# Performance work log

Measured on AMD Instinct MI355X. Metric: run time of the kernel, lower is better.

## Reference

```python
import jax, jax.numpy as jnp
import numpy as np
import math

B, S, D, NCLS, H = 32, 2048, 512, 2, 16
HD = D // H
KSIZE = 19


def setup_inputs() -> dict:
    key = jax.random.key(0)
    ks = jax.random.split(key, 20)
    f32 = jnp.float32
    s = 1.0 / math.sqrt(D)
    inp = {}
    inp['x'] = jax.random.normal(ks[0], (B, S, D), dtype=f32)
    # wave params [2, D, 1]: row 0 = scale (1 + randn), row 1 = shift
    inp['wave1'] = jnp.concatenate([1.0 + jax.random.normal(ks[1], (1, D, 1), f32), jax.random.normal(ks[2], (1, D, 1), f32)], axis=0)
    inp['wave2'] = jnp.concatenate([1.0 + jax.random.normal(ks[3], (1, D, 1), f32), jnp.zeros((1, D, 1), f32)], axis=0)
    inp['wave3'] = jnp.concatenate([1.0 + jax.random.normal(ks[4], (1, D, 1), f32), jnp.zeros((1, D, 1), f32)], axis=0)
    inp['Wp1'] = jax.random.normal(ks[5], (D, D), f32) * s   # WaveletEncoding.proj_1
    inp['bp1'] = jnp.zeros((D,), f32)
    inp['cls_token'] = jax.random.normal(ks[6], (1, NCLS, D), f32) * 0.02
    inp['ln1_g'] = jnp.ones((D,), f32)
    inp['ln1_b'] = jnp.zeros((D,), f32)
    inp['Wq'] = jax.random.normal(ks[7], (D, D), f32) * s      # no bias (qkv_bias=False)
    inp['Wkv'] = jax.random.normal(ks[8], (D, 2 * D), f32) * s
    inp['Wproj'] = jax.random.normal(ks[9], (D, D), f32) * s
    inp['bproj'] = jnp.zeros((D,), f32)
    inp['ln2_g'] = jnp.ones((D,), f32)
    inp['ln2_b'] = jnp.zeros((D,), f32)
    inp['Wc1'] = jax.random.normal(ks[10], (D, D), f32) * s
    inp['bc1'] = jnp.zeros((D,), f32)
    inp['Wc2'] = jax.random.normal(ks[11], (D, 1), f32) * s
    inp['bc2'] = jnp.zeros((1,), f32)
    return inp


def _layernorm(x, g, b, eps=1e-5):
    m = jnp.mean(x, axis=-1, keepdims=True)
    v = jnp.mean((x - m) ** 2, axis=-1, keepdims=True)
    return (x - m) / jnp.sqrt(v + eps) * g + b


def _mexican_hat(wave):
    # wave: [2, D, 1] -> kernel [D, KSIZE]
    scale, shift = wave[0], wave[1]                      # [D, 1]
    half = (KSIZE - 1) // 2
    xs = jnp.linspace(-half, half, KSIZE, dtype=jnp.float32)  # [KSIZE]
    xg = xs[None, :] - shift                             # [D, KSIZE]
    C = 2.0 / (3.0 ** 0.5 * np.pi ** 0.25)
    u = xg / scale
    return C * (1.0 - u ** 2) * jnp.exp(-0.5 * u ** 2) / jnp.sqrt(jnp.abs(scale))


def _dwconv(xc, kern):
    # xc [B, D, S], kern [D, KSIZE]; depthwise 'same' conv (groups=D)
    return jax.lax.conv_general_dilated(
        xc, kern[:, None, :], window_strides=(1,), padding='SAME',
        dimension_numbers=('NCH', 'OIH', 'NCH'), feature_group_count=D)


def _forward(x, wave1, wave2, wave3, Wp1, bp1, cls_token, ln1_g, ln1_b,
             Wq, Wkv, Wproj, bproj, ln2_g, ln2_b, Wc1, bc1, Wc2, bc2):
    # Wavelet positional encoding
    xc = jnp.transpose(x, (0, 2, 1))                     # [B, D, S]
    pos = _dwconv(xc, _mexican_hat(wave1)) + _dwconv(xc, _mexican_hat(wave2)) + _dwconv(xc, _mexican_hat(wave3))
    x = x + jnp.transpose(pos, (0, 2, 1)) @ Wp1 + bp1    # [B, S, D]
    # MIL pooling: layernorm on encoder tokens, sigmoid cross-attention
    xn = _layernorm(x, ln1_g, ln1_b)
    cls = jnp.broadcast_to(cls_token, (x.shape[0], NCLS, D))
    q = (cls @ Wq).reshape(-1, NCLS, H, HD).transpose(0, 2, 1, 3)        # [B, H, N, hd]
    kv = (xn @ Wkv).reshape(-1, S, 2, H, HD).transpose(2, 0, 3, 1, 4)    # [2, B, H, S, hd]
    k, v = kv[0], kv[1]
    scale = HD ** (-0.5)
    scores = jnp.einsum('bhnd,bhsd->bhns', q, k) * scale - math.log(S)   # -log(S) bias
    attn = jax.nn.sigmoid(scores)                                        # sigmoid, not softmax
    o = jnp.einsum('bhns,bhsd->bhnd', attn, v).transpose(0, 2, 1, 3).reshape(-1, NCLS, D)
    o = o @ Wproj + bproj
    # classifier head
    h = jax.nn.relu(_layernorm(o, ln2_g, ln2_b) @ Wc1 + bc1)
    logits = (h @ Wc2 + bc2)[..., 0]                                     # [B, NCLS]
    return logits, attn


def reference(x, wave1, wave2, wave3, Wp1, bp1, cls_token, ln1_g, ln1_b,
              Wq, Wkv, Wproj, bproj, ln2_g, ln2_b, Wc1, bc1, Wc2, bc2):
    return _forward(x, wave1, wave2, wave3, Wp1, bp1, cls_token, ln1_g, ln1_b,
                    Wq, Wkv, Wproj, bproj, ln2_g, ln2_b, Wc1, bc1, Wc2, bc2)
```

## Files before the change

### kernel.cpp

```cpp
#include <hip/hip_runtime.h>

#define SEQ 2048
#define DIM 512
#define NBATCH 32
#define NH 16
#define HDIM 32
#define NCLS 2

typedef __attribute__((ext_vector_type(8))) short short8;
typedef __attribute__((ext_vector_type(8))) unsigned short ushort8;
typedef __attribute__((ext_vector_type(4))) float f32x4;

__device__ __forceinline__ float b2f(unsigned short u){
  union { unsigned int i; float f; } v; v.i = ((unsigned int)u) << 16; return v.f;
}
__device__ __forceinline__ unsigned short f2b(float f){
  unsigned int x = __float_as_uint(f);
  unsigned int r = (x + 0x7fffu + ((x >> 16) & 1u)) >> 16;
  return (unsigned short)r;
}
__device__ __forceinline__ void gload16(const void* g, void* l){
  __builtin_amdgcn_global_load_lds((const __attribute__((address_space(1))) void*)g,
                                   (__attribute__((address_space(3))) void*)l, 16, 0, 0);
}

__global__ __launch_bounds__(256) void prep1_kernel(
    const float* __restrict__ w1, const float* __restrict__ w2, const float* __restrict__ w3,
    float* __restrict__ ksum,
    const float* __restrict__ cls, const float* __restrict__ Wq, float* __restrict__ qws,
    const float* __restrict__ Wp1, unsigned short* __restrict__ Wp1T,
    const float* __restrict__ Wkv, const float* __restrict__ g1, unsigned short* __restrict__ GvT){
  __shared__ unsigned short t[64][65];
  int bid = blockIdx.x;
  int tid = threadIdx.x;
  if (bid < 2){
    int d = bid * 256 + tid;
    const float C = 0.86732501f;
    float acc[19];
    #pragma unroll
    for (int i = 0; i < 19; ++i) acc[i] = 0.f;
    const float* waves[3] = { w1, w2, w3 };
    for (int tt = 0; tt < 3; ++tt){
      float scale = waves[tt][d];
      float shift = waves[tt][DIM + d];
      float inv = 1.f / scale;
      float amp = C * rsqrtf(fabsf(scale));
      #pragma unroll
      for (int i = 0; i < 19; ++i){
        float u = ((float)(i - 9) - shift) * inv;
        acc[i] += amp * (1.f - u * u) * expf(-0.5f * u * u);
      }
    }
    #pragma unroll
    for (int i = 0; i < 19; ++i) ksum[i * DIM + d] = acc[i];
  } else if (bid < 6){
    int idx = (bid - 2) * 256 + tid;
    int n = idx >> 9, c = idx & 511;
    float s = 0.f;
    for (int kd = 0; kd < DIM; ++kd)
      s = fmaf(cls[n * DIM + kd], Wq[(size_t)kd * DIM + c], s);
    qws[n * DIM + c] = s;
  } else if (bid < 70){
    int bx = bid - 6;
    int c0 = (bx & 7) * 64, r0 = (bx >> 3) * 64;
    #pragma unroll
    for (int i = 0; i < 16; ++i){
      int idx = i * 256 + tid;
      int r = idx >> 6, c = idx & 63;
      t[c][r] = f2b(Wp1[(size_t)(r0 + r) * 512 + c0 + c]);
    }
    __syncthreads();
    #pragma unroll
    for (int i = 0; i < 16; ++i){
      int idx = i * 256 + tid;
      int r = idx >> 6, c = idx & 63;
      Wp1T[(size_t)(c0 + r) * 512 + r0 + c] = t[r][c];
    }
  } else {
    int bx = bid - 70;
    int c0 = (bx & 7) * 64, r0 = (bx >> 3) * 64;
    #pragma unroll
    for (int i = 0; i < 16; ++i){
      int idx = i * 256 + tid;
      int r = idx >> 6, c = idx & 63;
      t[c][r] = f2b(Wkv[(size_t)(r0 + r) * 1024 + 512 + c0 + c] * g1[r0 + r]);
    }
    __syncthreads();
    #pragma unroll
    for (int i = 0; i < 16; ++i){
      int idx = i * 256 + tid;
      int r = idx >> 6, c = idx & 63;
      GvT[(size_t)(c0 + r) * 512 + r0 + c] = t[r][c];
    }
  }
}

__global__ __launch_bounds__(256) void prep2_kernel(const float* __restrict__ Wkv,
    const float* __restrict__ qws, const float* __restrict__ g1, const float* __restrict__ b1,
    unsigned short* __restrict__ AqT, float* __restrict__ gv, float* __restrict__ bv,
    float* __restrict__ ga, float* __restrict__ ba){
  const float SCALE = 0.17677669529663687f;
  const float LOGS  = 7.6246189861593985f;
  int bid = blockIdx.x;
  int tid = threadIdx.x;
  if (bid < 64){
    int idx = bid * 256 + tid;
    int hn = idx >> 9, d = idx & 511;
    int h = hn >> 1, n = hn & 1;
    float s = 0.f;
    #pragma unroll
    for (int hd = 0; hd < 32; ++hd)
      s = fmaf(Wkv[(size_t)d * 1024 + h * 32 + hd], qws[n * 512 + h * 32 + hd], s);
    AqT[hn * 512 + d] = f2b(SCALE * g1[d] * s);
  } else if (bid < 96){
    __shared__ float red[64];
    int hn = bid - 64;
    int h = hn >> 1, n = hn & 1;
    float s1 = 0.f, s2 = 0.f;
    #pragma unroll
    for (int dd = 0; dd < 2; ++dd){
      int d = tid + dd * 256;
      float inner = 0.f;
      #pragma unroll
      for (int hd = 0; hd < 32; ++hd)
        inner = fmaf(Wkv[(size_t)d * 1024 + h * 32 + hd], qws[n * 512 + h * 32 + hd], inner);
      s1 = fmaf(g1[d], inner, s1);
      s2 = fmaf(b1[d], inner, s2);
    }
    #pragma unroll
    for (int off = 32; off; off >>= 1){
      s1 += __shfl_xor(s1, off, 64);
      s2 += __shfl_xor(s2, off, 64);
    }
    int w = tid >> 6, lane = tid & 63;
    if (lane == 0){ red[w * 2] = s1; red[w * 2 + 1] = s2; }
    __syncthreads();
    if (tid == 0){
      float t1 = red[0] + red[2] + red[4] + red[6];
      float t2 = red[1] + red[3] + red[5] + red[7];
      ga[hn] = SCALE * t1;
      ba[hn] = SCALE * t2 - LOGS;
    }
  } else {
    int c = (bid - 96) * 256 + tid;
    float s1 = 0.f, s2 = 0.f;
    for (int d = 0; d < 512; ++d){
      float wv = Wkv[(size_t)d * 1024 + 512 + c];
      s1 = fmaf(g1[d], wv, s1);
      s2 = fmaf(b1[d], wv, s2);
    }
    gv[c] = s1; bv[c] = s2;
  }
}

__global__ __launch_bounds__(256) void conv_kernel(const float* __restrict__ X,
    const float* __restrict__ ksum, unsigned short* __restrict__ Pos){
  __shared__ float xs[34 * 256];
  int id = blockIdx.x;
  int id2 = (id & 7) * 1024 + (id >> 3);
  int b = id2 >> 8;
  int rem = id2 & 255;
  int strip = rem >> 1, half = rem & 1;
  int s0 = strip * 16, c0 = half * 256;
  int tid = threadIdx.x;
  const float* xb = X + ((size_t)b * SEQ) * DIM + c0;
  #pragma unroll
  for (int i = 0; i < 9; ++i){
    int g = i * 256 + tid;
    if (g < 2176){
      int row = g >> 6;
      int gc = g & 63;
      int s = s0 - 9 + row;
      int sc = s < 0 ? 0 : (s > SEQ - 1 ? SEQ - 1 : s);
      gload16(xb + (size_t)sc * DIM + gc * 4, &xs[row * 256 + gc * 4]);
    }
  }
  __syncthreads();
  if (strip == 0){
    #pragma unroll
    for (int i = 0; i < 9; ++i) xs[i * 256 + tid] = 0.f;
    __syncthreads();
  } else if (strip == 127){
    #pragma unroll
    for (int i = 25; i < 34; ++i) xs[i * 256 + tid] = 0.f;
    __syncthreads();
  }
  int d = tid;
  float kx[19];
  #pragma unroll
  for (int t = 0; t < 19; ++t) kx[t] = ksum[t * DIM + c0 + d];
  float ox[16];
  #pragma unroll
  for (int o = 0; o < 16; ++o) ox[o] = 0.f;
  #pragma unroll
  for (int w = 0; w < 34; ++w){
    float xv = xs[w * 256 + d];
    #pragma unroll
    for (int o = 0; o < 16; ++o){
      int t2 = w - o;
      if (t2 >= 0 && t2 < 19) ox[o] = fmaf(xv, kx[t2], ox[o]);
    }
  }
  #pragma unroll
  for (int o = 0; o < 16; ++o)
    Pos[((size_t)(b * SEQ + s0 + o)) * DIM + c0 + d] = f2b(ox[o]);
}

__global__ __launch_bounds__(512, 4) void gemm1_kernel(const unsigned short* __restrict__ A,
    const unsigned short* __restrict__ Bt, const float* __restrict__ Xres,
    const float* __restrict__ bias, unsigned short* __restrict__ Out,
    float* __restrict__ stat_part){
  __shared__ unsigned short lA[2 * 8192];
  __shared__ unsigned short lB[2 * 8192];
  __shared__ float sred[128][2][2];
  int tid = threadIdx.x;
  int w = tid >> 6, lane = tid & 63;
  int wm = w >> 1, wn = w & 1;
  int q = lane >> 4, cl = lane & 15;
  int id = blockIdx.x;
  int xcd = id & 7;
  int nch = (id >> 3) & 3;
  int mb  = ((id >> 5) << 3) | xcd;
  size_t mBase = (size_t)mb * 128;
  int nBase = nch * 128;

  auto stage = [&](int buf, int k0){
    #pragma unroll
    for (int p = 0; p < 2; ++p){
      int G = p * 512 + tid;
      int row = G >> 3;
      int c8 = (G & 7) ^ (row & 7);
      gload16(A + (mBase + row) * 512 + k0 + c8 * 8, &lA[buf * 8192 + G * 8]);
      gload16(Bt + (size_t)(nBase + row) * 512 + k0 + c8 * 8, &lB[buf * 8192 + G * 8]);
    }
  };

  f32x4 acc[2][4] = {};
  stage(0, 0);
  __syncthreads();
  int cur = 0;
  #pragma unroll
  for (int t = 0; t < 8; ++t){
    if (t < 7){
      stage(cur ^ 1, (t + 1) * 64);
      asm volatile("s_waitcnt vmcnt(4)" ::: "memory");
    } else {
      asm volatile("s_waitcnt vmcnt(0)" ::: "memory");
    }
    __builtin_amdgcn_s_barrier();
    const unsigned short* cA = &lA[cur * 8192];
    const unsigned short* cB = &lB[cur * 8192];
    #pragma unroll
    for (int kk = 0; kk < 2; ++kk){
      short8 af[2], bfr[4];
      #pragma unroll
      for (int m = 0; m < 2; ++m){
        int row = wm * 32 + m * 16 + cl;
        af[m] = *(const short8*)&cA[row * 64 + (((kk * 4 + q) ^ (row & 7)) * 8)];
      }
      #pragma unroll
      for (int n = 0; n < 4; ++n){
        int row = wn * 64 + n * 16 + cl;
        bfr[n] = *(const short8*)&cB[row * 64 + (((kk * 4 + q) ^ (row & 7)) * 8)];
      }
      #pragma unroll
      for (int m = 0; m < 2; ++m){
        #pragma unroll
        for (int n = 0; n < 4; ++n)
          acc[m][n] = __builtin_amdgcn_mfma_f32_16x16x32_bf16(af[m], bfr[n], acc[m][n], 0, 0, 0);
      }
    }
    asm volatile("s_waitcnt lgkmcnt(0)" ::: "memory");
    __builtin_amdgcn_s_barrier();
    cur ^= 1;
  }
  #pragma unroll
  for (int m = 0; m < 2; ++m){
    #pragma unroll
    for (int j = 0; j < 4; ++j){
      int rl = wm * 32 + m * 16 + q * 4 + j;
      size_t row = mBase + rl;
      float sm = 0.f, sq = 0.f;
      #pragma unroll
      for (int n = 0; n < 4; ++n){
        int col = nBase + wn * 64 + n * 16 + cl;
        float v = acc[m][n][j] + Xres[row * DIM + col] + bias[col];
        Out[row * DIM + col] = f2b(v);
        sm += v; sq += v * v;
      }
      #pragma unroll
      for (int off = 1; off < 16; off <<= 1){
        sm += __shfl_xor(sm, off, 64);
        sq += __shfl_xor(sq, off, 64);
      }
      if (cl == 0){ sred[rl][wn][0] = sm; sred[rl][wn][1] = sq; }
    }
  }
  __syncthreads();
  if (tid < 128){
    float sm = sred[tid][0][0] + sred[tid][1][0];
    float sq = sred[tid][0][1] + sred[tid][1][1];
    stat_part[((mBase + tid) * 4 + nch) * 2 + 0] = sm;
    stat_part[((mBase + tid) * 4 + nch) * 2 + 1] = sq;
  }
}

__global__ __launch_bounds__(512, 4) void stage2_kernel(
    const unsigned short* __restrict__ Y, const unsigned short* __restrict__ GvT,
    const unsigned short* __restrict__ AqT, const float* __restrict__ stat_part,
    const float* __restrict__ gv, const float* __restrict__ bv,
    const float* __restrict__ ga, const float* __restrict__ ba,
    float* __restrict__ aout, float* __restrict__ o_part){
  __shared__ __align__(16) char smem[74752];
  unsigned short* lA = (unsigned short*)smem;
  unsigned short* lB = (unsigned short*)(smem + 32768);
  float* stats = (float*)(smem + 73728);
  float* attn_lds = (float*)smem;
  float* o_red = (float*)(smem + 16896);
  int tid = threadIdx.x;
  int w = tid >> 6, lane = tid & 63;
  int wm = w >> 1, wn = w & 1;
  int q = lane >> 4, cl = lane & 15;
  int id = blockIdx.x;
  int xcd = id & 7;
  int nch = (id >> 3) & 3;
  int mb  = ((id >> 5) << 3) | xcd;
  size_t mBase = (size_t)mb * 128;
  int nBase = nch * 128;

  auto stage = [&](int buf, int k0){
    #pragma unroll
    for (int p = 0; p < 2; ++p){
      int G = p * 512 + tid;
      int row = G >> 3;
      int c8 = (G & 7) ^ (row & 7);
      gload16(Y + (mBase + row) * 512 + k0 + c8 * 8, &lA[buf * 8192 + G * 8]);
      gload16(GvT + (size_t)(nBase + row) * 512 + k0 + c8 * 8, &lB[buf * 10240 + G * 8]);
    }
    {
      int g = tid & 255;
      int row = 128 + (g >> 3);
      int c8 = (g & 7) ^ (row & 7);
      gload16(AqT + (size_t)(row - 128) * 512 + k0 + c8 * 8, &lB[buf * 10240 + (1024 + g) * 8]);
    }
  };

  stage(0, 0);
  if (tid < 128){
    float sm = 0.f, sq = 0.f;
    #pragma unroll
    for (int i = 0; i < 4; ++i){
      sm += stat_part[((mBase + tid) * 4 + i) * 2 + 0];
      sq += stat_part[((mBase + tid) * 4 + i) * 2 + 1];
    }
    float mean = sm * (1.f / 512.f);
    float var = sq * (1.f / 512.f) - mean * mean;
    stats[tid * 2 + 0] = mean;
    stats[tid * 2 + 1] = rsqrtf(var + 1e-5f);
  }
  __syncthreads();

  int hn = wn * 16 + cl;
  f32x4 acc[2][4] = {};
  f32x4 accs[2] = {};
  int cur = 0;
  #pragma unroll
  for (int t = 0; t < 8; ++t){
    if (t < 7){
      stage(cur ^ 1, (t + 1) * 64);
      asm volatile("s_waitcnt vmcnt(5)" ::: "memory");
    } else {
      asm volatile("s_waitcnt vmcnt(0)" ::: "memory");
    }
    __builtin_amdgcn_s_barrier();
    const unsigned short* cA = &lA[cur * 8192];
    const unsigned short* cB = &lB[cur * 10240];
    #pragma unroll
    for (int kk = 0; kk < 2; ++kk){
      short8 af[2], bfr[4], bq;
      {
        int row = 128 + hn;
        bq = *(const short8*)&cB[row * 64 + (((kk * 4 + q) ^ (row & 7)) * 8)];
      }
      #pragma unroll
      for (int m = 0; m < 2; ++m){
        int row = wm * 32 + m * 16 + cl;
        af[m] = *(const short8*)&cA[row * 64 + (((kk * 4 + q) ^ (row & 7)) * 8)];
      }
      #pragma unroll
      for (int n = 0; n < 4; ++n){
        int row = wn * 64 + n * 16 + cl;
        bfr[n] = *(const short8*)&cB[row * 64 + (((kk * 4 + q) ^ (row & 7)) * 8)];
      }
      #pragma unroll
      for (int m = 0; m < 2; ++m){
        #pragma unroll
        for (int n = 0; n < 4; ++n)
          acc[m][n] = __builtin_amdgcn_mfma_f32_16x16x32_bf16(af[m], bfr[n], acc[m][n], 0, 0, 0);
        accs[m] = __builtin_amdgcn_mfma_f32_16x16x32_bf16(af[m], bq, accs[m], 0, 0, 0);
      }
    }
    asm volatile("s_waitcnt lgkmcnt(0)" ::: "memory");
    __builtin_amdgcn_s_barrier();
    cur ^= 1;
  }
  float gav = ga[hn], bav = ba[hn];
  float gv4[4], bv4[4];
  #pragma unroll
  for (int n = 0; n < 4; ++n){
    int cg = nBase + wn * 64 + n * 16 + cl;
    gv4[n] = gv[cg]; bv4[n] = bv[cg];
  }
  int b = mb >> 4;
  int scb = (mb & 15) * 128;
  #pragma unroll
  for (int m = 0; m < 2; ++m){
    #pragma unroll
    for (int j = 0; j < 4; ++j){
      int rl = wm * 32 + m * 16 + q * 4 + j;
      float mu = stats[rl * 2 + 0], s = stats[rl * 2 + 1];
      float sc = s * accs[m][j] - s * mu * gav + bav;
      float at = 1.f / (1.f + expf(-sc));
      attn_lds[rl * 33 + hn] = at;
      if (nch == 0)
        aout[((size_t)(b * NH + (hn >> 1)) * NCLS + (hn & 1)) * SEQ + scb + rl] = at;
      #pragma unroll
      for (int n = 0; n < 4; ++n)
        acc[m][n][j] = s * acc[m][n][j] - s * mu * gv4[n] + bv4[n];
    }
  }
  __syncthreads();
  float o0[4] = {}, o1[4] = {};
  #pragma unroll
  for (int n = 0; n < 4; ++n){
    int cg = nBase + wn * 64 + n * 16 + cl;
    int h2 = ((cg >> 5) << 1);
    #pragma unroll
    for (int m = 0; m < 2; ++m){
      #pragma unroll
      for (int j = 0; j < 4; ++j){
        int rl = wm * 32 + m * 16 + q * 4 + j;
        float vv = acc[m][n][j];
        o0[n] = fmaf(attn_lds[rl * 33 + h2 + 0], vv, o0[n]);
        o1[n] = fmaf(attn_lds[rl * 33 + h2 + 1], vv, o1[n]);
      }
    }
  }
  #pragma unroll
  for (int n = 0; n < 4; ++n){
    o0[n] += __shfl_xor(o0[n], 16, 64);
    o0[n] += __shfl_xor(o0[n], 32, 64);
    o1[n] += __shfl_xor(o1[n], 16, 64);
    o1[n] += __shfl_xor(o1[n], 32, 64);
  }
  if (q == 0){
    #pragma unroll
    for (int n = 0; n < 4; ++n){
      int c = wn * 64 + n * 16 + cl;
      o_red[(0 * 4 + wm) * 128 + c] = o0[n];
      o_red[(1 * 4 + wm) * 128 + c] = o1[n];
    }
  }
  __syncthreads();
  if (tid < 256){
    int nn = tid >> 7, c = tid & 127;
    float v = o_red[(nn * 4 + 0) * 128 + c] + o_red[(nn * 4 + 1) * 128 + c]
            + o_red[(nn * 4 + 2) * 128 + c] + o_red[(nn * 4 + 3) * 128 + c];
    o_part[((size_t)mb * 2 + nn) * 512 + nBase + c] = v;
  }
}

__global__ __launch_bounds__(256) void head_kernel(const float* __restrict__ o_part,
    const float* __restrict__ Wproj, const float* __restrict__ bproj,
    const float* __restrict__ g2, const float* __restrict__ b2v,
    const float* __restrict__ Wc1, const float* __restrict__ bc1,
    const float* __restrict__ Wc2, const float* __restrict__ bc2,
    float* __restrict__ logits){
  __shared__ float orow[512];
  __shared__ float hrow[512];
  __shared__ float wred[8];
  __shared__ float wred2[4];
  int tid = threadIdx.x;
  int row = blockIdx.x;
  int b = row >> 1, nn = row & 1;
  for (int i = tid; i < 512; i += 256){
    float s = 0.f;
    const float* op = o_part + (((size_t)b * 16) * 2 + nn) * 512 + i;
    #pragma unroll
    for (int sc = 0; sc < 16; ++sc) s += op[(size_t)sc * 1024];
    orow[i] = s;
  }
  __syncthreads();
  int c0 = tid * 2;
  float a0 = 0.f, a1 = 0.f;
  for (int dd = 0; dd < DIM; ++dd){
    float ov = orow[dd];
    const float* wr = Wproj + (size_t)dd * DIM + c0;
    a0 = fmaf(ov, wr[0], a0);
    a1 = fmaf(ov, wr[1], a1);
  }
  a0 += bproj[c0]; a1 += bproj[c0 + 1];
  float sm = a0 + a1, sq = a0 * a0 + a1 * a1;
  #pragma unroll
  for (int off = 32; off; off >>= 1){
    sm += __shfl_xor(sm, off, 64);
    sq += __shfl_xor(sq, off, 64);
  }
  int w = tid >> 6, lane = tid & 63;
  if (lane == 0){ wred[w * 2] = sm; wred[w * 2 + 1] = sq; }
  __syncthreads();
  sm = wred[0] + wred[2] + wred[4] + wred[6];
  sq = wred[1] + wred[3] + wred[5] + wred[7];
  float mean = sm * (1.f / 512.f);
  float var = sq * (1.f / 512.f) - mean * mean;
  float rstd = rsqrtf(var + 1e-5f);
  hrow[c0]     = (a0 - mean) * rstd * g2[c0]     + b2v[c0];
  hrow[c0 + 1] = (a1 - mean) * rstd * g2[c0 + 1] + b2v[c0 + 1];
  __syncthreads();
  float h0 = 0.f, h1 = 0.f;
  for (int dd = 0; dd < DIM; ++dd){
    float lv = hrow[dd];
    const float* wr = Wc1 + (size_t)dd * DIM + c0;
    h0 = fmaf(lv, wr[0], h0);
    h1 = fmaf(lv, wr[1], h1);
  }
  h0 += bc1[c0]; h1 += bc1[c0 + 1];
  h0 = h0 > 0.f ? h0 : 0.f;
  h1 = h1 > 0.f ? h1 : 0.f;
  float p = h0 * Wc2[c0] + h1 * Wc2[c0 + 1];
  #pragma unroll
  for (int off = 32; off; off >>= 1) p += __shfl_xor(p, off, 64);
  if (lane == 0) wred2[w] = p;
  __syncthreads();
  if (tid == 0) logits[row] = wred2[0] + wred2[1] + wred2[2] + wred2[3] + bc2[0];
}

extern "C" void kernel_launch(void* const* d_in, const int* in_sizes, int n_in,
                              void* d_out, int out_size, void* d_ws, size_t ws_size,
                              hipStream_t stream) {
  const float* x     = (const float*)d_in[0];
  const float* wave1 = (const float*)d_in[1];
  const float* wave2 = (const float*)d_in[2];
  const float* wave3 = (const float*)d_in[3];
  const float* Wp1   = (const float*)d_in[4];
  const float* bp1   = (const float*)d_in[5];
  const float* cls   = (const float*)d_in[6];
  const float* ln1g  = (const float*)d_in[7];
  const float* ln1b  = (const float*)d_in[8];
  const float* Wq    = (const float*)d_in[9];
  const float* Wkv   = (const float*)d_in[10];
  const float* Wproj = (const float*)d_in[11];
  const float* bproj = (const float*)d_in[12];
  const float* ln2g  = (const float*)d_in[13];
  const float* ln2b  = (const float*)d_in[14];
  const float* Wc1   = (const float*)d_in[15];
  const float* bc1   = (const float*)d_in[16];
  const float* Wc2   = (const float*)d_in[17];
  const float* bc2   = (const float*)d_in[18];

  float* out = (float*)d_out;
  float* logits = out;
  float* attn   = out + 64;

  unsigned char* ws = (unsigned char*)d_ws;
  float* ksum           = (float*)(ws);
  float* qws            = (float*)(ws + (64u << 10));
  unsigned short* Wp1T  = (unsigned short*)(ws + (128u << 10));
  unsigned short* GvT   = (unsigned short*)(ws + (640u << 10));
  unsigned short* AqT   = (unsigned short*)(ws + (1152u << 10));
  float* gv             = (float*)(ws + (1248u << 10));
  float* bv             = (float*)(ws + (1252u << 10));
  float* ga             = (float*)(ws + (1256u << 10));
  float* ba             = (float*)(ws + (1260u << 10));
  float* o_part         = (float*)(ws + (1776u << 10));
  float* stat_part      = (float*)(ws + (4096u << 10));
  unsigned short* pos   = (unsigned short*)(ws + (8ull << 20));
  unsigned short* yb    = (unsigned short*)(ws + (72ull << 20));

  prep1_kernel<<<dim3(134), dim3(256), 0, stream>>>(wave1, wave2, wave3, ksum,
                                                    cls, Wq, qws, Wp1, Wp1T, Wkv, ln1g, GvT);
  prep2_kernel<<<dim3(98), dim3(256), 0, stream>>>(Wkv, qws, ln1g, ln1b, AqT, gv, bv, ga, ba);
  conv_kernel<<<dim3(8192), dim3(256), 0, stream>>>(x, ksum, pos);
  gemm1_kernel<<<dim3(2048), dim3(512), 0, stream>>>(pos, Wp1T, x, bp1, yb, stat_part);
  stage2_kernel<<<dim3(2048), dim3(512), 0, stream>>>(yb, GvT, AqT, stat_part,
                                                      gv, bv, ga, ba, attn, o_part);
  head_kernel<<<dim3(64), dim3(256), 0, stream>>>(o_part, Wproj, bproj, ln2g, ln2b,
                                                  Wc1, bc1, Wc2, bc2, logits);
}
```

Measured before the change: 271.2 us.

## Merge prep kernels and compute wavelet taps inside conv kernel

Folds the two preparation kernels into one launch. Each attention block now recomputes its own 32-element slice of the cls·Wq query instead of waiting for a separate kernel to write it. The wavelet kernel taps are now computed per thread inside the conv kernel, overlapping the staged x loads, so conv no longer depends on a prep kernel. This removes one kernel launch and its serial dependency, at the cost of redundant exp evaluations in every conv block and redundant query computation across prep blocks.

```diff
diff --git a/kernel.cpp b/kernel.cpp
--- a/kernel.cpp
+++ b/kernel.cpp
@@ -24,45 +24,22 @@
                                    (__attribute__((address_space(3))) void*)l, 16, 0, 0);
 }
 
-__global__ __launch_bounds__(256) void prep1_kernel(
-    const float* __restrict__ w1, const float* __restrict__ w2, const float* __restrict__ w3,
-    float* __restrict__ ksum,
-    const float* __restrict__ cls, const float* __restrict__ Wq, float* __restrict__ qws,
-    const float* __restrict__ Wp1, unsigned short* __restrict__ Wp1T,
-    const float* __restrict__ Wkv, const float* __restrict__ g1, unsigned short* __restrict__ GvT){
+__global__ __launch_bounds__(256) void prep_kernel(
+    const float* __restrict__ Wp1, const float* __restrict__ Wkv,
+    const float* __restrict__ g1, const float* __restrict__ b1,
+    const float* __restrict__ cls, const float* __restrict__ Wq,
+    unsigned short* __restrict__ Wp1T, unsigned short* __restrict__ GvT,
+    unsigned short* __restrict__ AqT, float* __restrict__ gv, float* __restrict__ bv,
+    float* __restrict__ ga, float* __restrict__ ba){
+  const float SCALE = 0.17677669529663687f;
+  const float LOGS  = 7.6246189861593985f;
+  __shared__ float qred[32][9];
+  __shared__ float q32[32];
   __shared__ unsigned short t[64][65];
   int bid = blockIdx.x;
   int tid = threadIdx.x;
-  if (bid < 2){
-    int d = bid * 256 + tid;
-    const float C = 0.86732501f;
-    float acc[19];
-    #pragma unroll
-    for (int i = 0; i < 19; ++i) acc[i] = 0.f;
-    const float* waves[3] = { w1, w2, w3 };
-    for (int tt = 0; tt < 3; ++tt){
-      float scale = waves[tt][d];
-      float shift = waves[tt][DIM + d];
-      float inv = 1.f / scale;
-      float amp = C * rsqrtf(fabsf(scale));
-      #pragma unroll
-      for (int i = 0; i < 19; ++i){
-        float u = ((float)(i - 9) - shift) * inv;
-        acc[i] += amp * (1.f - u * u) * expf(-0.5f * u * u);
-      }
-    }
-    #pragma unroll
-    for (int i = 0; i < 19; ++i) ksum[i * DIM + d] = acc[i];
-  } else if (bid < 6){
-    int idx = (bid - 2) * 256 + tid;
-    int n = idx >> 9, c = idx & 511;
-    float s = 0.f;
-    for (int kd = 0; kd < DIM; ++kd)
-      s = fmaf(cls[n * DIM + kd], Wq[(size_t)kd * DIM + c], s);
-    qws[n * DIM + c] = s;
-  } else if (bid < 70){
-    int bx = bid - 6;
-    int c0 = (bx & 7) * 64, r0 = (bx >> 3) * 64;
+  if (bid < 64){
+    int c0 = (bid & 7) * 64, r0 = (bid >> 3) * 64;
     #pragma unroll
     for (int i = 0; i < 16; ++i){
       int idx = i * 256 + tid;
@@ -76,8 +53,8 @@
       int r = idx >> 6, c = idx & 63;
       Wp1T[(size_t)(c0 + r) * 512 + r0 + c] = t[r][c];
     }
-  } else {
-    int bx = bid - 70;
+  } else if (bid < 128){
+    int bx = bid - 64;
     int c0 = (bx & 7) * 64, r0 = (bx >> 3) * 64;
     #pragma unroll
     for (int i = 0; i < 16; ++i){
@@ -92,57 +69,64 @@
       int r = idx >> 6, c = idx & 63;
       GvT[(size_t)(c0 + r) * 512 + r0 + c] = t[r][c];
     }
-  }
-}
-
-__global__ __launch_bounds__(256) void prep2_kernel(const float* __restrict__ Wkv,
-    const float* __restrict__ qws, const float* __restrict__ g1, const float* __restrict__ b1,
-    unsigned short* __restrict__ AqT, float* __restrict__ gv, float* __restrict__ bv,
-    float* __restrict__ ga, float* __restrict__ ba){
-  const float SCALE = 0.17677669529663687f;
-  const float LOGS  = 7.6246189861593985f;
-  int bid = blockIdx.x;
-  int tid = threadIdx.x;
-  if (bid < 64){
-    int idx = bid * 256 + tid;
-    int hn = idx >> 9, d = idx & 511;
+  } else if (bid < 224){
+    int hn = (bid < 192) ? ((bid - 128) >> 1) : (bid - 192);
     int h = hn >> 1, n = hn & 1;
-    float s = 0.f;
-    #pragma unroll
-    for (int hd = 0; hd < 32; ++hd)
-      s = fmaf(Wkv[(size_t)d * 1024 + h * 32 + hd], qws[n * 512 + h * 32 + hd], s);
-    AqT[hn * 512 + d] = f2b(SCALE * g1[d] * s);
-  } else if (bid < 96){
-    __shared__ float red[64];
-    int hn = bid - 64;
-    int h = hn >> 1, n = hn & 1;
-    float s1 = 0.f, s2 = 0.f;
-    #pragma unroll
-    for (int dd = 0; dd < 2; ++dd){
-      int d = tid + dd * 256;
-      float inner = 0.f;
+    {
+      int hd = tid >> 3, part = tid & 7;
+      float ps = 0.f;
+      #pragma unroll 8
+      for (int i = 0; i < 64; ++i){
+        int kd = part * 64 + i;
+        ps = fmaf(cls[n * 512 + kd], Wq[(size_t)kd * 512 + h * 32 + hd], ps);
+      }
+      qred[hd][part] = ps;
+      __syncthreads();
+      if (tid < 32){
+        float s = 0.f;
+        #pragma unroll
+        for (int p = 0; p < 8; ++p) s += qred[tid][p];
+        q32[tid] = s;
+      }
+      __syncthreads();
+    }
+    if (bid < 192){
+      int d = ((bid - 128) & 1) * 256 + tid;
+      float s = 0.f;
       #pragma unroll
       for (int hd = 0; hd < 32; ++hd)
-        inner = fmaf(Wkv[(size_t)d * 1024 + h * 32 + hd], qws[n * 512 + h * 32 + hd], inner);
-      s1 = fmaf(g1[d], inner, s1);
-      s2 = fmaf(b1[d], inner, s2);
-    }
-    #pragma unroll
-    for (int off = 32; off; off >>= 1){
-      s1 += __shfl_xor(s1, off, 64);
-      s2 += __shfl_xor(s2, off, 64);
-    }
-    int w = tid >> 6, lane = tid & 63;
-    if (lane == 0){ red[w * 2] = s1; red[w * 2 + 1] = s2; }
-    __syncthreads();
-    if (tid == 0){
-      float t1 = red[0] + red[2] + red[4] + red[6];
-      float t2 = red[1] + red[3] + red[5] + red[7];
-      ga[hn] = SCALE * t1;
-      ba[hn] = SCALE * t2 - LOGS;
+        s = fmaf(Wkv[(size_t)d * 1024 + h * 32 + hd], q32[hd], s);
+      AqT[hn * 512 + d] = f2b(SCALE * g1[d] * s);
+    } else {
+      __shared__ float red[8];
+      float s1 = 0.f, s2 = 0.f;
+      #pragma unroll
+      for (int dd = 0; dd < 2; ++dd){
+        int d = tid + dd * 256;
+        float inner = 0.f;
+        #pragma unroll
+        for (int hd = 0; hd < 32; ++hd)
+          inner = fmaf(Wkv[(size_t)d * 1024 + h * 32 + hd], q32[hd], inner);
+        s1 = fmaf(g1[d], inner, s1);
+        s2 = fmaf(b1[d], inner, s2);
+      }
+      #pragma unroll
+      for (int off = 32; off; off >>= 1){
+        s1 += __shfl_xor(s1, off, 64);
+        s2 += __shfl_xor(s2, off, 64);
+      }
+      int w = tid >> 6, lane = tid & 63;
+      if (lane == 0){ red[w * 2] = s1; red[w * 2 + 1] = s2; }
+      __syncthreads();
+      if (tid == 0){
+        float t1 = red[0] + red[2] + red[4] + red[6];
+        float t2 = red[1] + red[3] + red[5] + red[7];
+        ga[hn] = SCALE * t1;
+        ba[hn] = SCALE * t2 - LOGS;
+      }
     }
   } else {
-    int c = (bid - 96) * 256 + tid;
+    int c = (bid - 224) * 256 + tid;
     float s1 = 0.f, s2 = 0.f;
     for (int d = 0; d < 512; ++d){
       float wv = Wkv[(size_t)d * 1024 + 512 + c];
@@ -154,7 +138,8 @@
 }
 
 __global__ __launch_bounds__(256) void conv_kernel(const float* __restrict__ X,
-    const float* __restrict__ ksum, unsigned short* __restrict__ Pos){
+    const float* __restrict__ w1, const float* __restrict__ w2, const float* __restrict__ w3,
+    unsigned short* __restrict__ Pos){
   __shared__ float xs[34 * 256];
   int id = blockIdx.x;
   int id2 = (id & 7) * 1024 + (id >> 3);
@@ -175,6 +160,25 @@
       gload16(xb + (size_t)sc * DIM + gc * 4, &xs[row * 256 + gc * 4]);
     }
   }
+  int d = tid;
+  int dch = c0 + d;
+  float kx[19];
+  #pragma unroll
+  for (int i = 0; i < 19; ++i) kx[i] = 0.f;
+  const float C = 0.86732501f;
+  const float* waves[3] = { w1, w2, w3 };
+  #pragma unroll
+  for (int tt = 0; tt < 3; ++tt){
+    float scale = waves[tt][dch];
+    float shift = waves[tt][DIM + dch];
+    float inv = 1.f / scale;
+    float amp = C * rsqrtf(fabsf(scale));
+    #pragma unroll
+    for (int i = 0; i < 19; ++i){
+      float u = ((float)(i - 9) - shift) * inv;
+      kx[i] += amp * (1.f - u * u) * expf(-0.5f * u * u);
+    }
+  }
   __syncthreads();
   if (strip == 0){
     #pragma unroll
@@ -185,10 +189,6 @@
     for (int i = 25; i < 34; ++i) xs[i * 256 + tid] = 0.f;
     __syncthreads();
   }
-  int d = tid;
-  float kx[19];
-  #pragma unroll
-  for (int t = 0; t < 19; ++t) kx[t] = ksum[t * DIM + c0 + d];
   float ox[16];
   #pragma unroll
   for (int o = 0; o < 16; ++o) ox[o] = 0.f;
@@ -563,8 +563,6 @@
   float* attn   = out + 64;
 
   unsigned char* ws = (unsigned char*)d_ws;
-  float* ksum           = (float*)(ws);
-  float* qws            = (float*)(ws + (64u << 10));
   unsigned short* Wp1T  = (unsigned short*)(ws + (128u << 10));
   unsigned short* GvT   = (unsigned short*)(ws + (640u << 10));
   unsigned short* AqT   = (unsigned short*)(ws + (1152u << 10));
@@ -577,10 +575,9 @@
   unsigned short* pos   = (unsigned short*)(ws + (8ull << 20));
   unsigned short* yb    = (unsigned short*)(ws + (72ull << 20));
 
-  prep1_kernel<<<dim3(134), dim3(256), 0, stream>>>(wave1, wave2, wave3, ksum,
-                                                    cls, Wq, qws, Wp1, Wp1T, Wkv, ln1g, GvT);
-  prep2_kernel<<<dim3(98), dim3(256), 0, stream>>>(Wkv, qws, ln1g, ln1b, AqT, gv, bv, ga, ba);
-  conv_kernel<<<dim3(8192), dim3(256), 0, stream>>>(x, ksum, pos);
+  conv_kernel<<<dim3(8192), dim3(256), 0, stream>>>(x, wave1, wave2, wave3, pos);
+  prep_kernel<<<dim3(226), dim3(256), 0, stream>>>(Wp1, Wkv, ln1g, ln1b, cls, Wq,
+                                                   Wp1T, GvT, AqT, gv, bv, ga, ba);
   gemm1_kernel<<<dim3(2048), dim3(512), 0, stream>>>(pos, Wp1T, x, bp1, yb, stat_part);
   stage2_kernel<<<dim3(2048), dim3(512), 0, stream>>>(yb, GvT, AqT, stat_part,
                                                       gv, bv, ga, ba, attn, o_part);
```

Result: slower. 280.6 us (+3.5%).
